# Kernel tuning notes

Measured on AMD Instinct MI355X. Metric: run time of the kernel, lower is better.

Reference implementation:

```python
import jax, jax.numpy as jnp
import numpy as np
import math

B, S, D = 4, 2048, 1024
N_HEADS = 16
D_FF = 4096
T_DIM = 256
KEEP_RATIO = 0.7
EPS = 1e-5


def _layernorm(x):
    mu = jnp.mean(x, axis=-1, keepdims=True)
    var = jnp.mean((x - mu) ** 2, axis=-1, keepdims=True)
    return (x - mu) * jax.lax.rsqrt(var + EPS)


def _ada_ln(x, cond, W, b):
    # cond: (B, T_DIM); W: (2D, T_DIM)
    p = jax.nn.silu(cond) @ W.T + b            # (B, 2D)
    gamma, beta = jnp.split(p, 2, axis=-1)
    return _layernorm(x) * (1.0 + gamma[:, None, :]) + beta[:, None, :]


def _mha(h, in_w, in_b, out_w, out_b):
    b, s, d = h.shape
    hd = d // N_HEADS
    qkv = h @ in_w.T + in_b                     # (b, s, 3d)
    q, k, v = jnp.split(qkv, 3, axis=-1)
    def heads(t):
        return t.reshape(b, s, N_HEADS, hd).transpose(0, 2, 1, 3)
    q, k, v = heads(q), heads(k), heads(v)
    scores = jnp.einsum('bhqd,bhkd->bhqk', q, k) / math.sqrt(hd)
    attn = jax.nn.softmax(scores, axis=-1)
    o = jnp.einsum('bhqk,bhkd->bhqd', attn, v)  # (b, h, s, hd)
    o = o.transpose(0, 2, 1, 3).reshape(b, s, d)
    return o @ out_w.T + out_b


def setup_inputs() -> dict:
    key = jax.random.key(0)
    ks = jax.random.split(key, 24)
    sc = 0.02
    return {
        'x': jax.random.normal(ks[0], (B, S, D), jnp.float32),
        't_emb': jax.random.normal(ks[1], (B, T_DIM), jnp.float32),
        'tr_w1': jax.random.normal(ks[2], (32, D), jnp.float32) * sc,
        'tr_b1': jnp.zeros((32,), jnp.float32),
        'tr_w2': jax.random.normal(ks[3], (1, 32), jnp.float32) * sc,
        'tr_b2': jnp.zeros((1,), jnp.float32),
        'ln1_w': jax.random.normal(ks[4], (2 * D, T_DIM), jnp.float32) * sc,
        'ln1_b': jnp.zeros((2 * D,), jnp.float32),
        'ln2_w': jax.random.normal(ks[5], (2 * D, T_DIM), jnp.float32) * sc,
        'ln2_b': jnp.zeros((2 * D,), jnp.float32),
        'in_proj_w': jax.random.normal(ks[6], (3 * D, D), jnp.float32) * sc,
        'in_proj_b': jnp.zeros((3 * D,), jnp.float32),
        'out_w': jax.random.normal(ks[7], (D, D), jnp.float32) * sc,
        'out_b': jnp.zeros((D,), jnp.float32),
        'ffn_w1': jax.random.normal(ks[8], (D_FF, D), jnp.float32) * sc,
        'ffn_b1': jnp.zeros((D_FF,), jnp.float32),
        'ffn_w2': jax.random.normal(ks[9], (D, D_FF), jnp.float32) * sc,
        'ffn_b2': jnp.zeros((D,), jnp.float32),
        # torch inits gates to zero; use small randn so the block is non-trivial
        'gate_attn': jax.random.normal(ks[10], (1, 1, D), jnp.float32) * sc,
        'gate_ffn': jax.random.normal(ks[11], (1, 1, D), jnp.float32) * sc,
    }


def reference(x, t_emb, tr_w1, tr_b1, tr_w2, tr_b2, ln1_w, ln1_b, ln2_w, ln2_b,
              in_proj_w, in_proj_b, out_w, out_b, ffn_w1, ffn_b1, ffn_w2, ffn_b2,
              gate_attn, gate_ffn):
    b, s, d = x.shape
    num_keep = max(int(s * KEEP_RATIO), 1)

    # token importance on detached x (stop_gradient mirrors x.detach())
    xd = jax.lax.stop_gradient(x)
    imp = jax.nn.silu(xd @ tr_w1.T + tr_b1) @ tr_w2.T + tr_b2  # (b, s, 1)
    imp = imp[..., 0]
    _, idx = jax.lax.top_k(imp, num_keep)
    idx = jnp.sort(idx, axis=-1)                               # (b, num_keep)

    x_sel = jnp.take_along_axis(x, idx[..., None], axis=1)     # (b, k, d)

    h = _ada_ln(x_sel, t_emb, ln1_w, ln1_b)
    h = _mha(h, in_proj_w, in_proj_b, out_w, out_b)
    x_sel = x_sel + gate_attn * h

    h = _ada_ln(x_sel, t_emb, ln2_w, ln2_b)
    h = jax.nn.gelu(h @ ffn_w1.T + ffn_b1, approximate=False) @ ffn_w2.T + ffn_b2
    x_sel = x_sel + gate_ffn * h

    batch_idx = jnp.arange(b)[:, None]
    return x.at[batch_idx, idx].set(x_sel)
```

## Files before the change

kernel.cpp:

```cpp
#include <hip/hip_runtime.h>
#include <hip/hip_bf16.h>
#include <cmath>
#include <cstdint>

typedef __bf16 bf16;
typedef __bf16 bf16x8 __attribute__((ext_vector_type(8)));
typedef __bf16 bf16x4 __attribute__((ext_vector_type(4)));
typedef float  f32x4  __attribute__((ext_vector_type(4)));

constexpr int B_   = 4;
constexpr int S_   = 2048;
constexpr int D_   = 1024;
constexpr int H_   = 16;
constexpr int DFF_ = 4096;
constexpr int TD_  = 256;
constexpr int KEEP = 1433;
constexpr int M_TOT = B_ * KEEP;
constexpr int MPAD  = 5888;
constexpr int QT64  = (KEEP + 63) / 64;
constexpr int NKV   = (KEEP + 63) / 64;
constexpr float EPS = 1e-5f;
constexpr float QSCALE = 0.18033688011112042f;

__device__ __forceinline__ f32x4 mfma16(bf16x8 a, bf16x8 b, f32x4 c) {
  return __builtin_amdgcn_mfma_f32_16x16x32_bf16(a, b, c, 0, 0, 0);
}

#define GLOAD_LDS(gp, lp)                                                     \
  __builtin_amdgcn_global_load_lds(                                           \
      (const __attribute__((address_space(1))) void*)(gp),                    \
      (__attribute__((address_space(3))) void*)(lp), 16, 0, 0)

__global__ __launch_bounds__(256) void k_impgemv(
    const float* __restrict__ x, const float* __restrict__ w1,
    double* __restrict__ hidden)
{
  const int lane = threadIdx.x & 63, w = threadIdx.x >> 6;
  const int tok0 = blockIdx.x * 16 + w * 4;
  const int u0 = blockIdx.y * 8;
  const float* xb = x + (size_t)tok0 * D_ + lane * 4;
  const float* wb = w1 + (size_t)u0 * D_ + lane * 4;
  double acc[4][8] = {};
#pragma unroll 2
  for (int c = 0; c < D_; c += 256) {
    float4 xv[4], wv[8];
#pragma unroll
    for (int i = 0; i < 4; ++i)
      xv[i] = *(const float4*)(xb + (size_t)i * D_ + c);
#pragma unroll
    for (int u = 0; u < 8; ++u)
      wv[u] = *(const float4*)(wb + (size_t)u * D_ + c);
#pragma unroll
    for (int i = 0; i < 4; ++i)
#pragma unroll
      for (int u = 0; u < 8; ++u) {
        acc[i][u] += (double)xv[i].x * (double)wv[u].x;
        acc[i][u] += (double)xv[i].y * (double)wv[u].y;
        acc[i][u] += (double)xv[i].z * (double)wv[u].z;
        acc[i][u] += (double)xv[i].w * (double)wv[u].w;
      }
  }
#pragma unroll
  for (int i = 0; i < 4; ++i)
#pragma unroll
    for (int u = 0; u < 8; ++u) {
      double s = acc[i][u];
      for (int o = 32; o > 0; o >>= 1) s += __shfl_xor(s, o);
      acc[i][u] = s;
    }
  if (lane == 0) {
#pragma unroll
    for (int i = 0; i < 4; ++i)
#pragma unroll
      for (int u = 0; u < 8; ++u)
        hidden[(size_t)(tok0 + i) * 32 + u0 + u] = acc[i][u];
  }
}

__global__ __launch_bounds__(256) void k_imptail(
    const double* __restrict__ hidden, const float* __restrict__ b1,
    const float* __restrict__ w2, const float* __restrict__ b2,
    double* __restrict__ imp)
{
  const int tok = blockIdx.x * 256 + threadIdx.x;
  const double* hp = hidden + (size_t)tok * 32;
  double r = 0.0;
#pragma unroll
  for (int u = 0; u < 32; ++u) {
    double s = hp[u] + (double)b1[u];
    double sv = s / (1.0 + exp(-s));
    r += sv * (double)w2[u];
  }
  imp[tok] = r + (double)b2[0];
}

__global__ __launch_bounds__(256) void k_rank(const double* __restrict__ imp,
                                              int* __restrict__ rank)
{
  const int b = blockIdx.x >> 5;
  const int seg = blockIdx.x & 31;
  __shared__ double vals[S_];
  const double* ib = imp + (size_t)b * S_;
  for (int i = threadIdx.x; i < S_ / 2; i += 256)
    ((double2*)vals)[i] = ((const double2*)ib)[i];
  __syncthreads();
  const int tl = threadIdx.x >> 2;
  const int part = threadIdx.x & 3;
  const int s = seg * 64 + tl;
  const double v = vals[s];
  int cnt = 0;
  for (int j = part * 512; j < (part + 1) * 512; ++j) {
    double u = vals[j];
    cnt += (u > v) || (u == v && j < s);
  }
  cnt += __shfl_xor(cnt, 1);
  cnt += __shfl_xor(cnt, 2);
  if (part == 0) rank[b * S_ + s] = cnt;
}

__global__ __launch_bounds__(256) void k_compact(const int* __restrict__ rank,
                                                 int* __restrict__ idx)
{
  const int b = blockIdx.x;
  __shared__ int wcnt[4];
  __shared__ int base_s;
  if (threadIdx.x == 0) base_s = 0;
  __syncthreads();
  const int t = threadIdx.x, lane = t & 63, w = t >> 6;
  for (int c = 0; c < S_ / 256; ++c) {
    const int s = c * 256 + t;
    const bool kept = rank[b * S_ + s] < KEEP;
    unsigned long long m = __ballot(kept);
    int piw = __popcll(m & ((1ull << lane) - 1ull));
    if (lane == 0) wcnt[w] = __popcll(m);
    __syncthreads();
    int off = base_s;
    for (int i = 0; i < w; ++i) off += wcnt[i];
    if (kept) idx[b * KEEP + off + piw] = s;
    __syncthreads();
    if (t == 0) base_s += wcnt[0] + wcnt[1] + wcnt[2] + wcnt[3];
    __syncthreads();
  }
}

__global__ __launch_bounds__(256) void k_condproj(
    const float* __restrict__ temb, const float* __restrict__ W,
    const float* __restrict__ bias, float* __restrict__ p)
{
  const int gw = (int)((blockIdx.x * 256 + threadIdx.x) >> 6);
  const int lane = threadIdx.x & 63;
  const int b = gw >> 11;
  const int row = gw & 2047;
  const float* te = temb + (size_t)b * TD_;
  const float* wr = W + (size_t)row * TD_;
  float acc = 0.f;
  for (int i = lane; i < TD_; i += 64) {
    float c = te[i];
    acc += (c / (1.f + __expf(-c))) * wr[i];
  }
  for (int o = 32; o > 0; o >>= 1) acc += __shfl_down(acc, o);
  if (lane == 0) p[(size_t)b * 2 * D_ + row] = acc + bias[row];
}

__global__ void k_f2b(const float* __restrict__ src, bf16* __restrict__ dst, int n4)
{
  int i = blockIdx.x * 256 + threadIdx.x;
  if (i < n4) {
    float4 v = ((const float4*)src)[i];
    bf16x4 o = {(bf16)v.x, (bf16)v.y, (bf16)v.z, (bf16)v.w};
    ((bf16x4*)dst)[i] = o;
  }
}

__global__ __launch_bounds__(256) void k_adaln(
    const float* __restrict__ xsrc, const int* __restrict__ idx,
    const float* __restrict__ p, bf16* __restrict__ hout)
{
  const int r = blockIdx.x, t = threadIdx.x;
  bf16* orow = hout + (size_t)r * D_;
  if (r >= M_TOT) {
    bf16x4 z = {(bf16)0.f, (bf16)0.f, (bf16)0.f, (bf16)0.f};
    ((bf16x4*)orow)[t] = z;
    return;
  }
  const int b = r / KEEP, j = r - b * KEEP;
  const int s = idx[b * KEEP + j];
  const float* xr = xsrc + ((size_t)(b * S_ + s)) * D_;
  float4 v = ((const float4*)xr)[t];
  __shared__ float red[8];
  float sum = v.x + v.y + v.z + v.w;
  for (int o = 32; o > 0; o >>= 1) sum += __shfl_down(sum, o);
  const int lane = t & 63, w = t >> 6;
  if (lane == 0) red[w] = sum;
  __syncthreads();
  const float mu = (red[0] + red[1] + red[2] + red[3]) * (1.f / D_);
  const float dx = v.x - mu, dy = v.y - mu, dz = v.z - mu, dw = v.w - mu;
  float vs = dx * dx + dy * dy + dz * dz + dw * dw;
  for (int o = 32; o > 0; o >>= 1) vs += __shfl_down(vs, o);
  if (lane == 0) red[4 + w] = vs;
  __syncthreads();
  const float rstd = rsqrtf((red[4] + red[5] + red[6] + red[7]) * (1.f / D_) + EPS);
  const float* gp = p + (size_t)b * 2 * D_;
  float4 g  = ((const float4*)gp)[t];
  float4 be = ((const float4*)(gp + D_))[t];
  bf16x4 o;
  o[0] = (bf16)(dx * rstd * (1.f + g.x) + be.x);
  o[1] = (bf16)(dy * rstd * (1.f + g.y) + be.y);
  o[2] = (bf16)(dz * rstd * (1.f + g.z) + be.z);
  o[3] = (bf16)(dw * rstd * (1.f + g.w) + be.w);
  ((bf16x4*)orow)[t] = o;
}

template <int BN, int MODE>
__global__ __launch_bounds__(256) void k_gemm(
    const bf16* __restrict__ A, const bf16* __restrict__ W,
    const float* __restrict__ bias, bf16* __restrict__ Cbf,
    const float* __restrict__ gate, const int* __restrict__ idx,
    float* __restrict__ resid, int N, int K, int gn)
{
  constexpr int WN = BN / 2;
  constexpr int NJ = WN / 16;
  __shared__ bf16 As[2][128 * 64];
  __shared__ bf16 Ws[2][BN * 64];
  const int t = threadIdx.x, lane = t & 63;
  const int w = t >> 6, wr = w >> 1, wc = w & 1;
  const int fr = lane & 15, fq = lane >> 4;

  const int nwg = gridDim.x, orig = blockIdx.x;
  const int q8 = nwg >> 3, r8 = nwg & 7;
  const int xc = orig & 7, pos = orig >> 3;
  const int wgid = (xc < r8 ? xc * (q8 + 1) : r8 * (q8 + 1) + (xc - r8) * q8) + pos;
  const int bm = wgid / gn, bn = wgid - bm * gn;

  const bf16* Ab = A + (size_t)bm * 128 * K;
  const bf16* Wb = W + (size_t)bn * BN * K;

  auto stage = [&](int buf, int kt) {
    const int ko = kt * 64;
#pragma unroll
    for (int it = 0; it < 4; ++it) {
      const int e = it * 256 + t;
      const int row = e >> 3, pc = e & 7;
      const int lc = pc ^ (row & 7);
      GLOAD_LDS(Ab + (size_t)row * K + ko + lc * 8, &As[buf][0] + e * 8);
    }
#pragma unroll
    for (int it = 0; it < BN / 32; ++it) {
      const int e = it * 256 + t;
      const int row = e >> 3, pc = e & 7;
      const int lc = pc ^ (row & 7);
      GLOAD_LDS(Wb + (size_t)row * K + ko + lc * 8, &Ws[buf][0] + e * 8);
    }
  };

  f32x4 acc[4][NJ] = {};
  stage(0, 0);
  const int nkt = K >> 6;
  int cur = 0;
  for (int kt = 0; kt < nkt; ++kt) {
    __syncthreads();
    if (kt + 1 < nkt) stage(cur ^ 1, kt + 1);
    const char* Al = (const char*)&As[cur][0];
    const char* Wl = (const char*)&Ws[cur][0];
#pragma unroll
    for (int kk = 0; kk < 2; ++kk) {
      bf16x8 af[4], wf[NJ];
#pragma unroll
      for (int i = 0; i < 4; ++i)
        af[i] = *(const bf16x8*)(Al + (wr * 64 + i * 16 + fr) * 128 +
                                 (((kk * 4 + fq) ^ (fr & 7)) << 4));
#pragma unroll
      for (int j = 0; j < NJ; ++j)
        wf[j] = *(const bf16x8*)(Wl + (wc * WN + j * 16 + fr) * 128 +
                                 (((kk * 4 + fq) ^ (fr & 7)) << 4));
#pragma unroll
      for (int i = 0; i < 4; ++i)
#pragma unroll
        for (int j = 0; j < NJ; ++j)
          acc[i][j] = mfma16(af[i], wf[j], acc[i][j]);
    }
    cur ^= 1;
  }

#pragma unroll
  for (int i = 0; i < 4; ++i) {
#pragma unroll
    for (int j = 0; j < NJ; ++j) {
#pragma unroll
      for (int r = 0; r < 4; ++r) {
        const int m = bm * 128 + wr * 64 + i * 16 + fq * 4 + r;
        const int n = bn * BN + wc * WN + j * 16 + fr;
        float v = acc[i][j][r] + bias[n];
        if (MODE == 0) {
          if (n < D_) v *= QSCALE;
          Cbf[(size_t)m * N + n] = (bf16)v;
        } else if (MODE == 1) {
          float gl = 0.5f * v * (1.f + erff(v * 0.70710678118654752f));
          Cbf[(size_t)m * N + n] = (bf16)gl;
        } else {
          if (m < M_TOT) {
            const int b = m / KEEP, jj = m - b * KEEP;
            const int s = idx[b * KEEP + jj];
            resid[((size_t)(b * S_ + s)) * D_ + n] += gate[n] * v;
          }
        }
      }
    }
  }
}

__global__ __launch_bounds__(256) void k_attn(const bf16* __restrict__ qkv,
                                              bf16* __restrict__ out)
{
  __shared__ bf16 Klds[2][64 * 64];
  __shared__ bf16 Vlds[2][64 * 64];

  const int t = threadIdx.x;
  const int lane = t & 63, w = t >> 6;
  const int fr = lane & 15, fq = lane >> 4;
  const int qt = blockIdx.x, h = blockIdx.y, b = blockIdx.z;
  const size_t rowbase = (size_t)b * KEEP;
  const size_t RS = 3 * D_;
  const bf16* kbase = qkv + rowbase * RS + D_ + h * 64;
  const bf16* vbase = qkv + rowbase * RS + 2 * D_ + h * 64;

  const int wq0 = qt * 64 + w * 16;
  const int qrow = min(wq0 + fr, KEEP - 1);
  const bf16* qp = qkv + (rowbase + qrow) * RS + h * 64 + fq * 8;
  const bf16x8 qf0 = *(const bf16x8*)qp;
  const bf16x8 qf1 = *(const bf16x8*)(qp + 32);

  f32x4 o[4] = {};
  float mrow = -INFINITY, lrow = 0.f;

  const int p0 = t, p1 = 256 + t;
  auto kaddr = [&](int p, int kv) {
    const int row = p >> 3, c8p = p & 7;
    const int c8 = c8p ^ ((row & 7) ^ (row >> 3));
    const int gr = min(kv + row, KEEP - 1);
    return kbase + (size_t)gr * RS + c8 * 8;
  };
  auto vaddr = [&](int p, int kv) {
    const int db = p >> 7, ksub = (p >> 3) & 15, jr = (p >> 1) & 3,
              c8lo = p & 1;
    const int vrow = ksub * 4 + jr, vc8 = db * 2 + c8lo;
    const int gr = min(kv + vrow, KEEP - 1);
    return vbase + (size_t)gr * RS + vc8 * 8;
  };
  const bf16* kp0 = kaddr(p0, 0);
  const bf16* kp1 = kaddr(p1, 0);
  const bf16* vp0 = vaddr(p0, 0);
  const bf16* vp1 = vaddr(p1, 0);

  auto stage_fast = [&](int buf) {
    GLOAD_LDS(kp0, &Klds[buf][0] + p0 * 8);
    GLOAD_LDS(kp1, &Klds[buf][0] + p1 * 8);
    GLOAD_LDS(vp0, &Vlds[buf][0] + p0 * 8);
    GLOAD_LDS(vp1, &Vlds[buf][0] + p1 * 8);
    kp0 += 64 * RS; kp1 += 64 * RS; vp0 += 64 * RS; vp1 += 64 * RS;
  };
  auto stage_last = [&](int buf, int kv) {
    GLOAD_LDS(kaddr(p0, kv), &Klds[buf][0] + p0 * 8);
    GLOAD_LDS(kaddr(p1, kv), &Klds[buf][0] + p1 * 8);
    GLOAD_LDS(vaddr(p0, kv), &Vlds[buf][0] + p0 * 8);
    GLOAD_LDS(vaddr(p1, kv), &Vlds[buf][0] + p1 * 8);
  };

  stage_fast(0);
  int cur = 0;

  const unsigned vbase_lds0 =
      (unsigned)(size_t)(__attribute__((address_space(3))) bf16*)&Vlds[0][0];
  const unsigned vbase_lds1 =
      (unsigned)(size_t)(__attribute__((address_space(3))) bf16*)&Vlds[1][0];

  for (int ti = 0; ti < NKV; ++ti) {
    const int kv = ti * 64;
    __syncthreads();
    if (ti < NKV - 2) stage_fast(cur ^ 1);
    else if (ti == NKV - 2) stage_last(cur ^ 1, kv + 64);

    const char* Kl = (const char*)&Klds[cur][0];

    f32x4 sc[4];
    __builtin_amdgcn_s_setprio(1);
#pragma unroll
    for (int f = 0; f < 4; ++f) {
      const int row = ((f >> 1) << 5) + ((fr >> 2) << 3) + ((f & 1) << 1) +
                      (fr & 1) + (((fr >> 1) & 1) << 2);
      const int swz = (row & 7) ^ (row >> 3);
      const bf16x8 kf0 = *(const bf16x8*)(Kl + row * 128 + ((fq ^ swz) << 4));
      const bf16x8 kf1 =
          *(const bf16x8*)(Kl + row * 128 + (((fq ^ 4) ^ swz) << 4));
      f32x4 s = {0.f, 0.f, 0.f, 0.f};
      s = mfma16(kf0, qf0, s);
      s = mfma16(kf1, qf1, s);
      sc[f] = s;
    }
    __builtin_amdgcn_s_setprio(0);

    if (ti == NKV - 1) {
#pragma unroll
      for (int f = 0; f < 4; ++f)
#pragma unroll
        for (int r = 0; r < 4; ++r) {
          const int kl = ((f >> 1) << 5) + (fq << 3) + ((f & 1) << 1) +
                         (r & 1) + ((r >> 1) << 2);
          if (kv + kl >= KEEP) sc[f][r] = -INFINITY;
        }
    }
    float mx = sc[0][0];
#pragma unroll
    for (int f = 0; f < 4; ++f)
#pragma unroll
      for (int r = 0; r < 4; ++r) mx = fmaxf(mx, sc[f][r]);
    mx = fmaxf(mx, __shfl_xor(mx, 16));
    mx = fmaxf(mx, __shfl_xor(mx, 32));

    const bool noresc = __all(mx <= mrow + 8.f);
    const float mnew = noresc ? mrow : fmaxf(mrow, mx);
    float ps = 0.f;
    bf16 pe[4][4];
#pragma unroll
    for (int f = 0; f < 4; ++f)
#pragma unroll
      for (int r = 0; r < 4; ++r) {
        const float pv = exp2f(sc[f][r] - mnew);
        ps += pv;
        pe[f][r] = (bf16)pv;
      }
    ps += __shfl_xor(ps, 16);
    ps += __shfl_xor(ps, 32);
    if (!noresc) {
      const float fac = exp2f(mrow - mnew);
      lrow *= fac;
#pragma unroll
      for (int db = 0; db < 4; ++db) {
        o[db][0] *= fac; o[db][1] *= fac; o[db][2] *= fac; o[db][3] *= fac;
      }
      mrow = mnew;
    }
    lrow += ps;

    const bf16x8 pb[2] = {
        {pe[0][0], pe[0][1], pe[1][0], pe[1][1],
         pe[0][2], pe[0][3], pe[1][2], pe[1][3]},
        {pe[2][0], pe[2][1], pe[3][0], pe[3][1],
         pe[2][2], pe[2][3], pe[3][2], pe[3][3]}};
    const unsigned vb =
        (cur ? vbase_lds1 : vbase_lds0) + ((unsigned)fq << 7);
#pragma unroll
    for (int c = 0; c < 2; ++c) {
      const unsigned addr = vb + c * 1024;
      bf16x4 t0, t1, t2, t3, t4, t5, t6, t7;
      asm volatile(
          "ds_read_b64_tr_b16 %0, %8 offset:0\n\t"
          "ds_read_b64_tr_b16 %1, %8 offset:128\n\t"
          "ds_read_b64_tr_b16 %2, %8 offset:2048\n\t"
          "ds_read_b64_tr_b16 %3, %8 offset:2176\n\t"
          "ds_read_b64_tr_b16 %4, %8 offset:4096\n\t"
          "ds_read_b64_tr_b16 %5, %8 offset:4224\n\t"
          "ds_read_b64_tr_b16 %6, %8 offset:6144\n\t"
          "ds_read_b64_tr_b16 %7, %8 offset:6272\n\t"
          "s_waitcnt lgkmcnt(0)"
          : "=&v"(t0), "=&v"(t1), "=&v"(t2), "=&v"(t3),
            "=&v"(t4), "=&v"(t5), "=&v"(t6), "=&v"(t7)
          : "v"(addr));
      const bf16x8 vf0 = __builtin_shufflevector(t0, t1, 0, 1, 2, 3, 4, 5, 6, 7);
      const bf16x8 vf1 = __builtin_shufflevector(t2, t3, 0, 1, 2, 3, 4, 5, 6, 7);
      const bf16x8 vf2 = __builtin_shufflevector(t4, t5, 0, 1, 2, 3, 4, 5, 6, 7);
      const bf16x8 vf3 = __builtin_shufflevector(t6, t7, 0, 1, 2, 3, 4, 5, 6, 7);
      __builtin_amdgcn_s_setprio(1);
      o[0] = mfma16(vf0, pb[c], o[0]);
      o[1] = mfma16(vf1, pb[c], o[1]);
      o[2] = mfma16(vf2, pb[c], o[2]);
      o[3] = mfma16(vf3, pb[c], o[3]);
      __builtin_amdgcn_s_setprio(0);
    }
    cur ^= 1;
  }

  const int q = wq0 + fr;
  if (q < KEEP) {
    const float inv = 1.f / lrow;
#pragma unroll
    for (int db = 0; db < 4; ++db) {
      bf16x4 wv = {(bf16)(o[db][0] * inv), (bf16)(o[db][1] * inv),
                   (bf16)(o[db][2] * inv), (bf16)(o[db][3] * inv)};
      *(bf16x4*)(out + (rowbase + q) * (size_t)D_ + h * 64 + db * 16 + fq * 4) =
          wv;
    }
  }
}

extern "C" void kernel_launch(void* const* d_in, const int* in_sizes, int n_in,
                              void* d_out, int out_size, void* d_ws, size_t ws_size,
                              hipStream_t stream)
{
  (void)in_sizes; (void)n_in; (void)out_size; (void)ws_size;
  const float* x      = (const float*)d_in[0];
  const float* t_emb  = (const float*)d_in[1];
  const float* tr_w1  = (const float*)d_in[2];
  const float* tr_b1  = (const float*)d_in[3];
  const float* tr_w2  = (const float*)d_in[4];
  const float* tr_b2  = (const float*)d_in[5];
  const float* ln1_w  = (const float*)d_in[6];
  const float* ln1_b  = (const float*)d_in[7];
  const float* ln2_w  = (const float*)d_in[8];
  const float* ln2_b  = (const float*)d_in[9];
  const float* in_w   = (const float*)d_in[10];
  const float* in_b   = (const float*)d_in[11];
  const float* out_w  = (const float*)d_in[12];
  const float* out_b  = (const float*)d_in[13];
  const float* f1_w   = (const float*)d_in[14];
  const float* f1_b   = (const float*)d_in[15];
  const float* f2_w   = (const float*)d_in[16];
  const float* f2_b   = (const float*)d_in[17];
  const float* gate_a = (const float*)d_in[18];
  const float* gate_f = (const float*)d_in[19];

  char* ws = (char*)d_ws;
  size_t off = 0;
  auto alloc = [&](size_t bytes) -> char* {
    char* p = ws + off;
    off = (off + bytes + 255) & ~(size_t)255;
    return p;
  };
  double* imp  = (double*)alloc((size_t)B_ * S_ * 8);
  double* hid  = (double*)alloc((size_t)B_ * S_ * 32 * 8);
  int* rank    = (int*)alloc((size_t)B_ * S_ * 4);
  int* idx     = (int*)alloc((size_t)B_ * KEEP * 4);
  float* p1    = (float*)alloc((size_t)B_ * 2 * D_ * 4);
  float* p2    = (float*)alloc((size_t)B_ * 2 * D_ * 4);
  bf16* w_in   = (bf16*)alloc((size_t)3 * D_ * D_ * 2);
  bf16* w_out  = (bf16*)alloc((size_t)D_ * D_ * 2);
  bf16* w_f1   = (bf16*)alloc((size_t)DFF_ * D_ * 2);
  bf16* w_f2   = (bf16*)alloc((size_t)D_ * DFF_ * 2);
  bf16* h_bf   = (bf16*)alloc((size_t)MPAD * D_ * 2);
  bf16* big    = (bf16*)alloc((size_t)MPAD * (3 * D_ + D_) * 2);
  bf16* qkv    = big;
  bf16* attn   = big + (size_t)MPAD * 3 * D_;
  bf16* ffn1   = big;

  hipMemcpyAsync(d_out, x, (size_t)B_ * S_ * D_ * 4, hipMemcpyDeviceToDevice, stream);

  k_impgemv<<<dim3(B_ * S_ / 16, 4), 256, 0, stream>>>(x, tr_w1, hid);
  k_imptail<<<B_ * S_ / 256, 256, 0, stream>>>(hid, tr_b1, tr_w2, tr_b2, imp);
  k_rank<<<B_ * 32, 256, 0, stream>>>(imp, rank);
  k_compact<<<B_, 256, 0, stream>>>(rank, idx);

  k_condproj<<<(B_ * 2 * D_) / 4, 256, 0, stream>>>(t_emb, ln1_w, ln1_b, p1);
  k_condproj<<<(B_ * 2 * D_) / 4, 256, 0, stream>>>(t_emb, ln2_w, ln2_b, p2);

  k_f2b<<<(3 * D_ * D_ / 4 + 255) / 256, 256, 0, stream>>>(in_w, w_in, 3 * D_ * D_ / 4);
  k_f2b<<<(D_ * D_ / 4 + 255) / 256, 256, 0, stream>>>(out_w, w_out, D_ * D_ / 4);
  k_f2b<<<(DFF_ * D_ / 4 + 255) / 256, 256, 0, stream>>>(f1_w, w_f1, DFF_ * D_ / 4);
  k_f2b<<<(DFF_ * D_ / 4 + 255) / 256, 256, 0, stream>>>(f2_w, w_f2, DFF_ * D_ / 4);

  k_adaln<<<MPAD, 256, 0, stream>>>(x, idx, p1, h_bf);
  k_gemm<128, 0><<<46 * 24, 256, 0, stream>>>(
      h_bf, w_in, in_b, qkv, nullptr, nullptr, nullptr, 3 * D_, D_, 24);
  k_attn<<<dim3(QT64, H_, B_), 256, 0, stream>>>(qkv, attn);
  k_gemm<64, 2><<<46 * 16, 256, 0, stream>>>(
      attn, w_out, out_b, nullptr, gate_a, idx, (float*)d_out, D_, D_, 16);
  k_adaln<<<MPAD, 256, 0, stream>>>((const float*)d_out, idx, p2, h_bf);
  k_gemm<128, 1><<<46 * 32, 256, 0, stream>>>(
      h_bf, w_f1, f1_b, ffn1, nullptr, nullptr, nullptr, DFF_, D_, 32);
  k_gemm<64, 2><<<46 * 16, 256, 0, stream>>>(
      ffn1, w_f2, f2_b, nullptr, gate_f, idx, (float*)d_out, D_, DFF_, 16);
}
```

Baseline: 458.3 us.

## Fuse importance kernels, batch small launches, and hoist GEMM staging pointers

Merges the importance GEMV and its SiLU/projection tail into one kernel, which removes the double-precision hidden buffer round trip. The two condition-projection launches and the four weight-conversion launches each become a single launch that picks its source by index. Inside the GEMM, per-thread global load pointers are computed once and advanced each k-tile instead of being recomputed. The residual-scatter epilogue now looks up the row index once per row rather than once per element. The fused importance kernel gives up the 4-way split over hidden units, so it launches a quarter as many blocks and each block runs a serial loop.

```diff
diff --git a/kernel.cpp b/kernel.cpp
--- a/kernel.cpp
+++ b/kernel.cpp
@@ -31,67 +31,53 @@
       (const __attribute__((address_space(1))) void*)(gp),                    \
       (__attribute__((address_space(3))) void*)(lp), 16, 0, 0)
 
-__global__ __launch_bounds__(256) void k_impgemv(
+__global__ __launch_bounds__(256) void k_importance(
     const float* __restrict__ x, const float* __restrict__ w1,
-    double* __restrict__ hidden)
+    const float* __restrict__ b1, const float* __restrict__ w2,
+    const float* __restrict__ b2, double* __restrict__ imp)
 {
   const int lane = threadIdx.x & 63, w = threadIdx.x >> 6;
   const int tok0 = blockIdx.x * 16 + w * 4;
-  const int u0 = blockIdx.y * 8;
   const float* xb = x + (size_t)tok0 * D_ + lane * 4;
-  const float* wb = w1 + (size_t)u0 * D_ + lane * 4;
-  double acc[4][8] = {};
+  double r[4] = {};
+  for (int u0 = 0; u0 < 32; u0 += 8) {
+    const float* wb = w1 + (size_t)u0 * D_ + lane * 4;
+    double acc[4][8] = {};
 #pragma unroll 2
-  for (int c = 0; c < D_; c += 256) {
-    float4 xv[4], wv[8];
+    for (int c = 0; c < D_; c += 256) {
+      float4 xv[4], wv[8];
+#pragma unroll
+      for (int i = 0; i < 4; ++i)
+        xv[i] = *(const float4*)(xb + (size_t)i * D_ + c);
+#pragma unroll
+      for (int u = 0; u < 8; ++u)
+        wv[u] = *(const float4*)(wb + (size_t)u * D_ + c);
+#pragma unroll
+      for (int i = 0; i < 4; ++i)
+#pragma unroll
+        for (int u = 0; u < 8; ++u) {
+          acc[i][u] += (double)xv[i].x * (double)wv[u].x;
+          acc[i][u] += (double)xv[i].y * (double)wv[u].y;
+          acc[i][u] += (double)xv[i].z * (double)wv[u].z;
+          acc[i][u] += (double)xv[i].w * (double)wv[u].w;
+        }
+    }
 #pragma unroll
     for (int i = 0; i < 4; ++i)
-      xv[i] = *(const float4*)(xb + (size_t)i * D_ + c);
-#pragma unroll
-    for (int u = 0; u < 8; ++u)
-      wv[u] = *(const float4*)(wb + (size_t)u * D_ + c);
+#pragma unroll
+      for (int u = 0; u < 8; ++u) {
+        double s = acc[i][u];
+        for (int o = 32; o > 0; o >>= 1) s += __shfl_xor(s, o);
+        const double h = s + (double)b1[u0 + u];
+        const double sv = h / (1.0 + exp(-h));
+        r[i] += sv * (double)w2[u0 + u];
+      }
+  }
+  if (lane == 0) {
 #pragma unroll
     for (int i = 0; i < 4; ++i)
-#pragma unroll
-      for (int u = 0; u < 8; ++u) {
-        acc[i][u] += (double)xv[i].x * (double)wv[u].x;
-        acc[i][u] += (double)xv[i].y * (double)wv[u].y;
-        acc[i][u] += (double)xv[i].z * (double)wv[u].z;
-        acc[i][u] += (double)xv[i].w * (double)wv[u].w;
-      }
-  }
-#pragma unroll
-  for (int i = 0; i < 4; ++i)
-#pragma unroll
-    for (int u = 0; u < 8; ++u) {
-      double s = acc[i][u];
-      for (int o = 32; o > 0; o >>= 1) s += __shfl_xor(s, o);
-      acc[i][u] = s;
-    }
-  if (lane == 0) {
-#pragma unroll
-    for (int i = 0; i < 4; ++i)
-#pragma unroll
-      for (int u = 0; u < 8; ++u)
-        hidden[(size_t)(tok0 + i) * 32 + u0 + u] = acc[i][u];
-  }
-}
-
-__global__ __launch_bounds__(256) void k_imptail(
-    const double* __restrict__ hidden, const float* __restrict__ b1,
-    const float* __restrict__ w2, const float* __restrict__ b2,
-    double* __restrict__ imp)
-{
-  const int tok = blockIdx.x * 256 + threadIdx.x;
-  const double* hp = hidden + (size_t)tok * 32;
-  double r = 0.0;
-#pragma unroll
-  for (int u = 0; u < 32; ++u) {
-    double s = hp[u] + (double)b1[u];
-    double sv = s / (1.0 + exp(-s));
-    r += sv * (double)w2[u];
-  }
-  imp[tok] = r + (double)b2[0];
+      imp[tok0 + i] = r[i] + (double)b2[0];
+  }
 }
 
 __global__ __launch_bounds__(256) void k_rank(const double* __restrict__ imp,
@@ -144,11 +130,16 @@
 }
 
 __global__ __launch_bounds__(256) void k_condproj(
-    const float* __restrict__ temb, const float* __restrict__ W,
-    const float* __restrict__ bias, float* __restrict__ p)
-{
-  const int gw = (int)((blockIdx.x * 256 + threadIdx.x) >> 6);
+    const float* __restrict__ temb,
+    const float* __restrict__ W1, const float* __restrict__ b1f,
+    float* __restrict__ p1,
+    const float* __restrict__ W2, const float* __restrict__ b2f,
+    float* __restrict__ p2)
+{
+  int gw = (int)((blockIdx.x * 256 + threadIdx.x) >> 6);
   const int lane = threadIdx.x & 63;
+  const float* W = W1; const float* bias = b1f; float* p = p1;
+  if (gw >= 8192) { gw -= 8192; W = W2; bias = b2f; p = p2; }
   const int b = gw >> 11;
   const int row = gw & 2047;
   const float* te = temb + (size_t)b * TD_;
@@ -162,14 +153,20 @@
   if (lane == 0) p[(size_t)b * 2 * D_ + row] = acc + bias[row];
 }
 
-__global__ void k_f2b(const float* __restrict__ src, bf16* __restrict__ dst, int n4)
-{
-  int i = blockIdx.x * 256 + threadIdx.x;
-  if (i < n4) {
-    float4 v = ((const float4*)src)[i];
-    bf16x4 o = {(bf16)v.x, (bf16)v.y, (bf16)v.z, (bf16)v.w};
-    ((bf16x4*)dst)[i] = o;
-  }
+__global__ void k_f2b(const float* __restrict__ s0, const float* __restrict__ s1,
+                      const float* __restrict__ s2, const float* __restrict__ s3,
+                      bf16* __restrict__ d0, bf16* __restrict__ d1,
+                      bf16* __restrict__ d2, bf16* __restrict__ d3)
+{
+  const int g = blockIdx.x * 256 + threadIdx.x;
+  const float* src; bf16* dst; int off;
+  if (g < 786432)       { src = s0; dst = d0; off = g; }
+  else if (g < 1048576) { src = s1; dst = d1; off = g - 786432; }
+  else if (g < 2097152) { src = s2; dst = d2; off = g - 1048576; }
+  else                  { src = s3; dst = d3; off = g - 2097152; }
+  float4 v = ((const float4*)src)[off];
+  bf16x4 o = {(bf16)v.x, (bf16)v.y, (bf16)v.z, (bf16)v.w};
+  ((bf16x4*)dst)[off] = o;
 }
 
 __global__ __launch_bounds__(256) void k_adaln(
@@ -220,6 +217,7 @@
 {
   constexpr int WN = BN / 2;
   constexpr int NJ = WN / 16;
+  constexpr int WIT = BN / 32;
   __shared__ bf16 As[2][128 * 64];
   __shared__ bf16 Ws[2][BN * 64];
   const int t = threadIdx.x, lane = t & 63;
@@ -235,31 +233,43 @@
   const bf16* Ab = A + (size_t)bm * 128 * K;
   const bf16* Wb = W + (size_t)bn * BN * K;
 
-  auto stage = [&](int buf, int kt) {
-    const int ko = kt * 64;
+  const bf16* pA[4];
+  const bf16* pW[WIT];
+#pragma unroll
+  for (int it = 0; it < 4; ++it) {
+    const int e = it * 256 + t;
+    const int row = e >> 3, pc = e & 7;
+    const int lc = pc ^ (row & 7);
+    pA[it] = Ab + (size_t)row * K + lc * 8;
+  }
+#pragma unroll
+  for (int it = 0; it < WIT; ++it) {
+    const int e = it * 256 + t;
+    const int row = e >> 3, pc = e & 7;
+    const int lc = pc ^ (row & 7);
+    pW[it] = Wb + (size_t)row * K + lc * 8;
+  }
+
+  auto stage = [&](int buf) {
 #pragma unroll
     for (int it = 0; it < 4; ++it) {
-      const int e = it * 256 + t;
-      const int row = e >> 3, pc = e & 7;
-      const int lc = pc ^ (row & 7);
-      GLOAD_LDS(Ab + (size_t)row * K + ko + lc * 8, &As[buf][0] + e * 8);
-    }
-#pragma unroll
-    for (int it = 0; it < BN / 32; ++it) {
-      const int e = it * 256 + t;
-      const int row = e >> 3, pc = e & 7;
-      const int lc = pc ^ (row & 7);
-      GLOAD_LDS(Wb + (size_t)row * K + ko + lc * 8, &Ws[buf][0] + e * 8);
+      GLOAD_LDS(pA[it], &As[buf][0] + (it * 256 + t) * 8);
+      pA[it] += 64;
+    }
+#pragma unroll
+    for (int it = 0; it < WIT; ++it) {
+      GLOAD_LDS(pW[it], &Ws[buf][0] + (it * 256 + t) * 8);
+      pW[it] += 64;
     }
   };
 
   f32x4 acc[4][NJ] = {};
-  stage(0, 0);
+  stage(0);
   const int nkt = K >> 6;
   int cur = 0;
   for (int kt = 0; kt < nkt; ++kt) {
     __syncthreads();
-    if (kt + 1 < nkt) stage(cur ^ 1, kt + 1);
+    if (kt + 1 < nkt) stage(cur ^ 1);
     const char* Al = (const char*)&As[cur][0];
     const char* Wl = (const char*)&Ws[cur][0];
 #pragma unroll
@@ -282,26 +292,40 @@
     cur ^= 1;
   }
 
-#pragma unroll
-  for (int i = 0; i < 4; ++i) {
-#pragma unroll
-    for (int j = 0; j < NJ; ++j) {
+  if (MODE == 2) {
+#pragma unroll
+    for (int i = 0; i < 4; ++i) {
 #pragma unroll
       for (int r = 0; r < 4; ++r) {
         const int m = bm * 128 + wr * 64 + i * 16 + fq * 4 + r;
-        const int n = bn * BN + wc * WN + j * 16 + fr;
-        float v = acc[i][j][r] + bias[n];
-        if (MODE == 0) {
-          if (n < D_) v *= QSCALE;
-          Cbf[(size_t)m * N + n] = (bf16)v;
-        } else if (MODE == 1) {
-          float gl = 0.5f * v * (1.f + erff(v * 0.70710678118654752f));
-          Cbf[(size_t)m * N + n] = (bf16)gl;
-        } else {
-          if (m < M_TOT) {
-            const int b = m / KEEP, jj = m - b * KEEP;
-            const int s = idx[b * KEEP + jj];
-            resid[((size_t)(b * S_ + s)) * D_ + n] += gate[n] * v;
+        if (m < M_TOT) {
+          const int b = m / KEEP, jj = m - b * KEEP;
+          const int s = idx[b * KEEP + jj];
+          float* rp = resid + ((size_t)(b * S_ + s)) * D_ + bn * BN + wc * WN + fr;
+          const float* gp = gate + bn * BN + wc * WN + fr;
+          const float* bp = bias + bn * BN + wc * WN + fr;
+#pragma unroll
+          for (int j = 0; j < NJ; ++j)
+            rp[j * 16] += gp[j * 16] * (acc[i][j][r] + bp[j * 16]);
+        }
+      }
+    }
+  } else {
+#pragma unroll
+    for (int i = 0; i < 4; ++i) {
+#pragma unroll
+      for (int j = 0; j < NJ; ++j) {
+#pragma unroll
+        for (int r = 0; r < 4; ++r) {
+          const int m = bm * 128 + wr * 64 + i * 16 + fq * 4 + r;
+          const int n = bn * BN + wc * WN + j * 16 + fr;
+          float v = acc[i][j][r] + bias[n];
+          if (MODE == 0) {
+            if (n < D_) v *= QSCALE;
+            Cbf[(size_t)m * N + n] = (bf16)v;
+          } else {
+            float gl = 0.5f * v * (1.f + erff(v * 0.70710678118654752f));
+            Cbf[(size_t)m * N + n] = (bf16)gl;
           }
         }
       }
@@ -527,7 +551,6 @@
     return p;
   };
   double* imp  = (double*)alloc((size_t)B_ * S_ * 8);
-  double* hid  = (double*)alloc((size_t)B_ * S_ * 32 * 8);
   int* rank    = (int*)alloc((size_t)B_ * S_ * 4);
   int* idx     = (int*)alloc((size_t)B_ * KEEP * 4);
   float* p1    = (float*)alloc((size_t)B_ * 2 * D_ * 4);
@@ -544,18 +567,12 @@
 
   hipMemcpyAsync(d_out, x, (size_t)B_ * S_ * D_ * 4, hipMemcpyDeviceToDevice, stream);
 
-  k_impgemv<<<dim3(B_ * S_ / 16, 4), 256, 0, stream>>>(x, tr_w1, hid);
-  k_imptail<<<B_ * S_ / 256, 256, 0, stream>>>(hid, tr_b1, tr_w2, tr_b2, imp);
+  k_importance<<<B_ * S_ / 16, 256, 0, stream>>>(x, tr_w1, tr_b1, tr_w2, tr_b2, imp);
   k_rank<<<B_ * 32, 256, 0, stream>>>(imp, rank);
   k_compact<<<B_, 256, 0, stream>>>(rank, idx);
 
-  k_condproj<<<(B_ * 2 * D_) / 4, 256, 0, stream>>>(t_emb, ln1_w, ln1_b, p1);
-  k_condproj<<<(B_ * 2 * D_) / 4, 256, 0, stream>>>(t_emb, ln2_w, ln2_b, p2);
-
-  k_f2b<<<(3 * D_ * D_ / 4 + 255) / 256, 256, 0, stream>>>(in_w, w_in, 3 * D_ * D_ / 4);
-  k_f2b<<<(D_ * D_ / 4 + 255) / 256, 256, 0, stream>>>(out_w, w_out, D_ * D_ / 4);
-  k_f2b<<<(DFF_ * D_ / 4 + 255) / 256, 256, 0, stream>>>(f1_w, w_f1, DFF_ * D_ / 4);
-  k_f2b<<<(DFF_ * D_ / 4 + 255) / 256, 256, 0, stream>>>(f2_w, w_f2, DFF_ * D_ / 4);
+  k_condproj<<<4096, 256, 0, stream>>>(t_emb, ln1_w, ln1_b, p1, ln2_w, ln2_b, p2);
+  k_f2b<<<12288, 256, 0, stream>>>(in_w, out_w, f1_w, f2_w, w_in, w_out, w_f1, w_f2);
 
   k_adaln<<<MPAD, 256, 0, stream>>>(x, idx, p1, h_bf);
   k_gemm<128, 0><<<46 * 24, 256, 0, stream>>>(
```

Measured after the change: 450.2 us. Within noise of the previous version (-1.8%).
